# Kernel optimization log

Hardware: AMD Instinct MI355X
Metric: run time of the kernel (lower is better)

## Reference

```python
import jax, jax.numpy as jnp
import numpy as np

B, H, W, D, C, K, ITERS = 16, 64, 64, 64, 16, 5, 4
EPS_LN = 1e-5

def _ln(x, g, b):
    m = x.mean(-1, keepdims=True)
    v = jnp.mean((x - m) ** 2, axis=-1, keepdims=True)
    return (x - m) / jnp.sqrt(v + EPS_LN) * g + b

def _build_grid(h, w):
    # (h, w, 2) with x in [-1,1] over width, y in [-1,1] over height
    y, x = jnp.meshgrid(jnp.linspace(-1.0, 1.0, h), jnp.linspace(-1.0, 1.0, w), indexing='ij')
    return jnp.stack([x, y], axis=-1)

def _forward(feat, feat_color, mask, slot_noise, slots_mu, slots_logsigma,
             w_grid, b_grid, w_k, w_v, ln_kv_g, ln_kv_b, w_mlp, b_mlp,
             ln_q_g, ln_q_b, w_q, w_ih, w_hh, b_ih, b_hh,
             ln_feat_g, ln_feat_b, ln_color_g, ln_color_b,
             ln_res_g, ln_res_b, w_res, b_res):
    b, h, w, d = feat.shape
    n = h * w
    k_slots = mask.shape[0]
    scale = d ** (-0.5)

    grid = _build_grid(h, w)  # (H, W, 2)

    # fg position: weighted mean of grid under mask -> (K, 2), broadcast to (B, K, 2)
    gm = grid.transpose(2, 0, 1)[None] * mask            # (K, 2, H, W)
    fg_pos = gm.sum((2, 3)) / (mask.sum((2, 3)) + 1e-5)  # (K, 2)
    fg_pos = jnp.broadcast_to(fg_pos[None], (b, k_slots, 2))

    feat_n = _ln(feat.reshape(b, n, d), ln_feat_g, ln_feat_b)                    # (B, N, D)
    featc_n = _ln(feat_color.reshape(b, n, feat_color.shape[-1]), ln_color_g, ln_color_b)

    slot = slots_mu + jnp.exp(slots_logsigma) * slot_noise  # (B, K, D)

    # k/v with relative positional grid embedding (fg_pos is constant across iters,
    # so k/v are iteration-invariant and computed once -- same math as the original loop)
    rel = grid[None, None] - fg_pos[:, :, None, None, :]        # (B, K, H, W, 2)
    rel4 = jnp.concatenate([rel, -rel], -1).reshape(b, k_slots, n, 4)
    grid_embed = rel4 @ w_grid.T + b_grid                       # (B, K, N, D)
    k = _ln(feat_n @ w_k.T[None] [0][None][0][None][0] if False else (feat_n @ w_k.T)[:, None] + grid_embed, ln_kv_g, ln_kv_b) @ w_mlp.T + b_mlp
    v = _ln((feat_n @ w_v.T)[:, None] + grid_embed, ln_kv_g, ln_kv_b) @ w_mlp.T + b_mlp

    attn = None
    for it in range(ITERS):
        prev = slot
        q = _ln(slot, ln_q_g, ln_q_b) @ w_q.T                         # (B, K, D)
        logits = jnp.einsum('bkd,bknd->bkn', q, k) * scale
        attn = jax.nn.softmax(logits, axis=-1)                        # (B, K, N)
        upd = jnp.einsum('bkn,bknd->bkd', attn, v)                    # (B, K, D)
        if it != ITERS - 1:
            # torch GRUCell
            x = upd.reshape(-1, d)
            hp = slot.reshape(-1, d)
            gi = x @ w_ih.T + b_ih
            gh = hp @ w_hh.T + b_hh
            i_r, i_z, i_n = jnp.split(gi, 3, axis=-1)
            h_r, h_z, h_n = jnp.split(gh, 3, axis=-1)
            r = jax.nn.sigmoid(i_r + h_r)
            z = jax.nn.sigmoid(i_z + h_z)
            nn_ = jnp.tanh(i_n + r * h_n)
            slot = ((1.0 - z) * nn_ + z * hp).reshape(b, k_slots, d)
            slot = _ln(slot, ln_res_g, ln_res_b) @ w_res.T + b_res + prev
        else:
            slot_color = jnp.einsum('bkn,bnc->bkc', attn, featc_n)
            slot = jnp.concatenate([slot, slot_color], axis=-1)       # (B, K, D+C)

    amin = attn.min(axis=2, keepdims=True)
    amax = attn.max(axis=2, keepdims=True)
    attn = (attn - amin) / (amax - amin + 1e-5)
    return slot, fg_pos, attn

def setup_inputs() -> dict:
    key = jax.random.key(0)
    ks = jax.random.split(key, 16)
    def rn(i, shape, s=0.02):
        return jax.random.normal(ks[i], shape, jnp.float32) * s
    return {
        'feat': jax.random.normal(ks[0], (B, H, W, D), jnp.float32),
        'feat_color': jax.random.normal(ks[1], (B, H, W, C), jnp.float32),
        'mask': jax.random.uniform(ks[2], (K, 1, H, W), jnp.float32),
        'slot_noise': jax.random.normal(ks[3], (B, K, D), jnp.float32),
        'slots_mu': rn(4, (1, 1, D), 1.0),
        'slots_logsigma': rn(5, (1, 1, D), 0.01),
        'w_grid': rn(6, (D, 4)), 'b_grid': jnp.zeros((D,), jnp.float32),
        'w_k': rn(7, (D, D)), 'w_v': rn(8, (D, D)),
        'ln_kv_g': jnp.ones((D,), jnp.float32), 'ln_kv_b': jnp.zeros((D,), jnp.float32),
        'w_mlp': rn(9, (D, D)), 'b_mlp': jnp.zeros((D,), jnp.float32),
        'ln_q_g': jnp.ones((D,), jnp.float32), 'ln_q_b': jnp.zeros((D,), jnp.float32),
        'w_q': rn(10, (D, D)),
        'w_ih': rn(11, (3 * D, D)), 'w_hh': rn(12, (3 * D, D)),
        'b_ih': jnp.zeros((3 * D,), jnp.float32), 'b_hh': jnp.zeros((3 * D,), jnp.float32),
        'ln_feat_g': jnp.ones((D,), jnp.float32), 'ln_feat_b': jnp.zeros((D,), jnp.float32),
        'ln_color_g': jnp.ones((C,), jnp.float32), 'ln_color_b': jnp.zeros((C,), jnp.float32),
        'ln_res_g': jnp.ones((D,), jnp.float32), 'ln_res_b': jnp.zeros((D,), jnp.float32),
        'w_res': rn(13, (D, D)), 'b_res': jnp.zeros((D,), jnp.float32),
    }

def reference(feat, feat_color, mask, slot_noise, slots_mu, slots_logsigma,
              w_grid, b_grid, w_k, w_v, ln_kv_g, ln_kv_b, w_mlp, b_mlp,
              ln_q_g, ln_q_b, w_q, w_ih, w_hh, b_ih, b_hh,
              ln_feat_g, ln_feat_b, ln_color_g, ln_color_b,
              ln_res_g, ln_res_b, w_res, b_res):
    return _forward(feat, feat_color, mask, slot_noise, slots_mu, slots_logsigma,
                    w_grid, b_grid, w_k, w_v, ln_kv_g, ln_kv_b, w_mlp, b_mlp,
                    ln_q_g, ln_q_b, w_q, w_ih, w_hh, b_ih, b_hh,
                    ln_feat_g, ln_feat_b, ln_color_g, ln_color_b,
                    ln_res_g, ln_res_b, w_res, b_res)
```

## Files before the change

kernel.cpp:

```cpp
#include <hip/hip_runtime.h>
#include <stdint.h>

#define B_ 16
#define H_ 64
#define W_ 64
#define D_ 64
#define C_ 16
#define K_ 5
#define N_ 4096
#define NC_ 32
#define CS_ 128
#define EPS 1e-5f

typedef __attribute__((ext_vector_type(8))) short bf16x8;
typedef __attribute__((ext_vector_type(4))) float f32x4;

__device__ __forceinline__ float wsum64(float v){
  #pragma unroll
  for(int o=1;o<64;o<<=1) v += __shfl_xor(v,o,64);
  return v;
}
__device__ __forceinline__ float wmax64(float v){
  #pragma unroll
  for(int o=1;o<64;o<<=1) v = fmaxf(v, __shfl_xor(v,o,64));
  return v;
}
__device__ __forceinline__ float wmin64(float v){
  #pragma unroll
  for(int o=1;o<64;o<<=1) v = fminf(v, __shfl_xor(v,o,64));
  return v;
}
__device__ __forceinline__ uint16_t f2bf(float f){
  uint32_t u = __float_as_uint(f);
  u += 0x7fffu + ((u>>16)&1u);
  return (uint16_t)(u>>16);
}

__global__ __launch_bounds__(256) void k_pre(
    const float* __restrict__ mask, const float* __restrict__ noise,
    const float* __restrict__ mu, const float* __restrict__ lsg,
    const float* __restrict__ wm, const float* __restrict__ bm, const float* __restrict__ lnkb,
    const float* __restrict__ wk, const float* __restrict__ wv, const float* __restrict__ lnfb,
    const float* __restrict__ wq, const float* __restrict__ lnqg, const float* __restrict__ lnqb,
    const float* __restrict__ wres, const float* __restrict__ bres,
    const float* __restrict__ lnrg, const float* __restrict__ lnrb,
    const float* __restrict__ wih, const float* __restrict__ whh,
    const float* __restrict__ wg, const float* __restrict__ bg,
    const float* __restrict__ lnfg, const float* __restrict__ lnkg,
    float* __restrict__ ws_fg, float* __restrict__ out_fg,
    float* __restrict__ bm2, float* __restrict__ fkb, float* __restrict__ fvb,
    float* __restrict__ qb, float* __restrict__ br2,
    float* __restrict__ wgx, float* __restrict__ wgy, float* __restrict__ gscal,
    float* __restrict__ wqpT, float* __restrict__ wrpT,
    float* __restrict__ wvT, float* __restrict__ wmT,
    float* __restrict__ gw, float* __restrict__ slot, float* __restrict__ out_slot,
    float* __restrict__ WQp, float* __restrict__ WCp, float* __restrict__ bq2p,
    float* __restrict__ uvp, float* __restrict__ vqp, float* __restrict__ cscp){
  __shared__ float M0[64][65];
  __shared__ float M1[64][65];
  __shared__ float M2[64][65];
  __shared__ float vtmp[4][64];
  int bid=blockIdx.x, tid=threadIdx.x;
  if(bid<5){
    int k=bid;
    float sm=0.f, sx=0.f, sy=0.f;
    for(int p=tid; p<H_*W_; p+=256){
      int i=p>>6, j=p&63;
      float m = mask[k*H_*W_ + p];
      float x = -1.f + (2.f/63.f)*j;
      float y = -1.f + (2.f/63.f)*i;
      sm+=m; sx+=m*x; sy+=m*y;
    }
    __shared__ float r0[4], r1[4], r2[4];
    int wid=tid>>6, lane=tid&63;
    sm=wsum64(sm); sx=wsum64(sx); sy=wsum64(sy);
    if(lane==0){ r0[wid]=sm; r1[wid]=sx; r2[wid]=sy; }
    __syncthreads();
    if(tid==0){
      float tm=r0[0]+r0[1]+r0[2]+r0[3];
      float tx=r1[0]+r1[1]+r1[2]+r1[3];
      float ty=r2[0]+r2[1]+r2[2]+r2[3];
      float px = tx/(tm+1e-5f), py = ty/(tm+1e-5f);
      ws_fg[k*2+0]=px; ws_fg[k*2+1]=py;
      for(int b=0;b<B_;b++){ out_fg[(b*K_+k)*2+0]=px; out_fg[(b*K_+k)*2+1]=py; }
    }
  } else if(bid==5){
    int sel=tid>>6, o=tid&63; float s=0.f;
    if(sel==0){ s=bm[o]; for(int d=0;d<64;d++) s+=lnkb[d]*wm[o*64+d]; bm2[o]=s; }
    else if(sel==1){ for(int d=0;d<64;d++) s+=lnqb[d]*wq[o*64+d]; qb[o]=0.125f*s; }
    else if(sel==2){ for(int d=0;d<64;d++) s+=lnrb[d]*wres[o*64+d]; br2[o]=s+bres[o]; }
    else { for(int d=0;d<64;d++) s+=lnfb[d]*wk[o*64+d]; fkb[o]=s; }
  } else if(bid==6){
    int wv4=tid>>6, l=tid&63;
    if(wv4==0){ float s=0.f; for(int d=0;d<64;d++) s+=lnfb[d]*wv[l*64+d]; fvb[l]=s; }
    else if(wv4==1){
      float4 w4 = *(const float4*)(wg + l*4);
      wgx[l]=w4.x-w4.z; wgy[l]=w4.y-w4.w;
    } else if(wv4==2){
      float4 w4 = *(const float4*)(wg + l*4);
      float wx=w4.x-w4.z, wy=w4.y-w4.w, bl=bg[l];
      float t;
      t=wsum64(wx);    if(l==0) gscal[0]=t*(1.f/64.f);
      t=wsum64(wy);    if(l==0) gscal[1]=t*(1.f/64.f);
      t=wsum64(bl);    if(l==0) gscal[2]=t*(1.f/64.f);
      t=wsum64(wx*wx); if(l==0) gscal[3]=t*(1.f/64.f);
      t=wsum64(wy*wy); if(l==0) gscal[4]=t*(1.f/64.f);
      t=wsum64(wx*wy); if(l==0) gscal[5]=t*(2.f/64.f);
      t=wsum64(wx*bl); if(l==0) gscal[6]=t*(2.f/64.f);
      t=wsum64(wy*bl); if(l==0) gscal[7]=t*(2.f/64.f);
      t=wsum64(bl*bl); if(l==0) gscal[8]=t*(1.f/64.f);
    } else {
      for(int j=l;j<B_*K_*16;j+=64){ int bk2=j>>4, cc2=j&15; out_slot[bk2*80+64+cc2]=0.f; }
    }
  } else if(bid<71){
    int i=(bid-7)*256+tid;
    int a=i>>12, r=i&4095, d=r>>6, o=r&63;
    if(a==0)      wqpT[r]=0.125f*lnqg[d]*wq[o*64+d];
    else if(a==1) wrpT[r]=lnrg[d]*wres[o*64+d];
    else if(a==2) wvT[r]=wv[o*64+d];
    else          wmT[r]=wm[o*64+d];
  } else if(bid<167){
    int i=(bid-71)*256+tid;
    int g6=i>>12, r=i&4095, d=r>>6, o=r&63;
    float v = (g6<3)? wih[(g6*64+o)*64+d] : whh[((g6-3)*64+o)*64+d];
    gw[g6*4096 + d*64 + o] = v;
  } else if(bid<187){
    int i=(bid-167)*256+tid;
    if(i<B_*K_*D_){ int d=i&63; slot[i]=mu[d]+expf(lsg[d])*noise[i]; }
  } else if(bid==187){
    for(int i=tid;i<4096;i+=256){ int r=i>>6,c2=i&63; M0[r][c2]=wq[i]; M1[r][c2]=wm[i]; }
    __syncthreads();
    if(tid<64){ float s=0.f; for(int d=0;d<64;d++) s+=lnqb[d]*M0[tid][d]; vtmp[0][tid]=0.125f*s; }
    else if(tid<128){ int c2=tid-64; float s=bm[c2]; for(int d=0;d<64;d++) s+=lnkb[d]*M1[c2][d]; vtmp[1][c2]=s; }
    else if(tid<192){ int o=tid-128; float s=0.f; for(int d=0;d<64;d++) s+=lnfb[d]*wk[o*64+d]; vtmp[2][o]=s; }
    __syncthreads();
    for(int i=tid;i<4096;i+=256){ int d=i>>6,e=i&63; float s=0.f;
      for(int c2=0;c2<64;c2++) s=fmaf(M0[c2][d], M1[c2][e], s);
      M2[d][e]=0.125f*lnqg[d]*s; }
    __syncthreads();
    if(tid<64){
      int e=tid; float s=0.f; for(int c2=0;c2<64;c2++) s=fmaf(vtmp[0][c2], M1[c2][e], s); vtmp[3][e]=s;
    } else if(tid<128){
      int d=tid-64; float s=0.f; for(int c2=0;c2<64;c2++) s=fmaf(M0[c2][d], vtmp[1][c2], s);
      vqp[4*64+d]=0.125f*lnqg[d]*s;
    }
    __syncthreads();
    for(int i=tid;i<4096;i+=256){ int e=i>>6,o=i&63; M0[e][o]=lnkg[e]*wk[i]; }
    __syncthreads();
    for(int i=tid;i<4096;i+=256){ int d=i>>6,o=i&63; float s=0.f;
      for(int e=0;e<64;e++) s=fmaf(M2[d][e], M0[e][o], s);
      WQp[i]=lnfg[o]*s; }
    if(tid<64){ int o=tid; float s=0.f;
      for(int e=0;e<64;e++) s=fmaf(vtmp[3][e], M0[e][o], s);
      bq2p[o]=lnfg[o]*s; }
    else if(tid<128){ int d=tid-64; float s1=0.f,sx=0.f,sy=0.f,s3=0.f;
      for(int e=0;e<64;e++){ float pe=M2[d][e]*lnkg[e];
        float gx_=wg[e*4]-wg[e*4+2], gy_=wg[e*4+1]-wg[e*4+3];
        s1+=pe; sx+=pe*gx_; sy+=pe*gy_; s3+=pe*(bg[e]+vtmp[2][e]); }
      vqp[0*64+d]=s1; vqp[1*64+d]=sx; vqp[2*64+d]=sy; vqp[3*64+d]=s3; }
    else if(tid==128){ float c0=0.f,c1=0.f,c2=0.f,c3=0.f,c4=0.f;
      for(int e=0;e<64;e++){ float qe=vtmp[3][e]*lnkg[e];
        float gx_=wg[e*4]-wg[e*4+2], gy_=wg[e*4+1]-wg[e*4+3];
        c0+=qe; c1+=qe*gx_; c2+=qe*gy_; c3+=qe*(bg[e]+vtmp[2][e]);
        c4+=vtmp[0][e]*vtmp[1][e]; }
      cscp[0]=c0; cscp[1]=c1; cscp[2]=c2; cscp[3]=c3; cscp[4]=c4; }
  } else {
    for(int i=tid;i<4096;i+=256){ int r=i>>6,c2=i&63; M0[r][c2]=wv[i]*lnkg[r]; M1[r][c2]=wm[i]; }
    __syncthreads();
    if(tid<64){ float s=0.f; const float* wr=wv+tid*64;
      for(int d=0;d<64;d++) s+=lnfb[d]*wr[d]; vtmp[0][tid]=s; }
    __syncthreads();
    for(int i=tid;i<4096;i+=256){ int d=i>>6,o=i&63; float s=0.f;
      for(int e=0;e<64;e++) s=fmaf(M0[e][d], M1[o][e], s);
      WCp[i]=lnfg[d]*s; }
    if(tid<64){ int o=tid; float s1=0.f,s2=0.f,s3=0.f,s4=0.f;
      for(int e=0;e<64;e++){ float we=lnkg[e]*M1[o][e];
        float gx_=wg[e*4]-wg[e*4+2], gy_=wg[e*4+1]-wg[e*4+3];
        s1+=we*(vtmp[0][e]+bg[e]); s2+=we*gx_; s3+=we*gy_; s4+=we; }
      uvp[0*64+o]=s1; uvp[1*64+o]=s2; uvp[2*64+o]=s3; uvp[3*64+o]=s4; }
  }
}

__global__ __launch_bounds__(256) void k_featln(const float* __restrict__ feat,
    const float* __restrict__ wk, const float* __restrict__ wv, const float* __restrict__ gf,
    const float* __restrict__ fkb, const float* __restrict__ fvb,
    const float* __restrict__ wgx, const float* __restrict__ wgy, const float* __restrict__ bg,
    const float* __restrict__ fc, const float* __restrict__ gc, const float* __restrict__ bc,
    uint16_t* __restrict__ Aout, float4* __restrict__ kstat, float4* __restrict__ vstat,
    float* __restrict__ fcn){
  int tid=threadIdx.x, wid=tid>>6, lane=tid&63;
  int q=lane>>4, c=lane&15;
  size_t row = (size_t)blockIdx.x*64 + wid*16 + c;
  const float* xp = feat + row*64;
  float x[16];
  *(float4*)&x[0]  = *(const float4*)(xp + q*8);
  *(float4*)&x[4]  = *(const float4*)(xp + q*8 + 4);
  *(float4*)&x[8]  = *(const float4*)(xp + 32 + q*8);
  *(float4*)&x[12] = *(const float4*)(xp + 36 + q*8);
  float s=0.f;
  #pragma unroll
  for(int i=0;i<16;i++) s+=x[i];
  s += __shfl_xor(s,16,64); s += __shfl_xor(s,32,64);
  float mean = s*(1.f/64.f);
  float v=0.f;
  #pragma unroll
  for(int i=0;i<16;i++){ float d=x[i]-mean; v+=d*d; }
  v += __shfl_xor(v,16,64); v += __shfl_xor(v,32,64);
  float rs = rsqrtf(v*(1.f/64.f)+EPS);
  float gl[16];
  *(float4*)&gl[0]  = *(const float4*)(gf + q*8);
  *(float4*)&gl[4]  = *(const float4*)(gf + q*8 + 4);
  *(float4*)&gl[8]  = *(const float4*)(gf + 32 + q*8);
  *(float4*)&gl[12] = *(const float4*)(gf + 36 + q*8);
  bf16x8 A0, A1;
  #pragma unroll
  for(int j=0;j<8;j++){
    A0[j] = (short)f2bf((x[j]  -mean)*rs);
    A1[j] = (short)f2bf((x[8+j]-mean)*rs);
  }
  *(bf16x8*)(Aout + row*64 + q*8) = A0;
  *(bf16x8*)(Aout + row*64 + 32 + q*8) = A1;
  float wgxl[4][4], wgyl[4][4], bgl[4][4];
  #pragma unroll
  for(int ot=0;ot<4;ot++){
    *(float4*)&wgxl[ot][0] = *(const float4*)(wgx + ot*16 + q*4);
    *(float4*)&wgyl[ot][0] = *(const float4*)(wgy + ot*16 + q*4);
    *(float4*)&bgl[ot][0]  = *(const float4*)(bg + ot*16 + q*4);
  }
  #pragma unroll
  for(int mat=0;mat<2;mat++){
    const float* w = mat? wv : wk;
    const float* fb = mat? fvb : fkb;
    float ss=0.f, s2=0.f, dx=0.f, dy=0.f, db=0.f;
    #pragma unroll
    for(int ot=0; ot<4; ot++){
      const float* wp = w + (size_t)(ot*16+c)*64 + q*8;
      bf16x8 W0, W1;
      #pragma unroll
      for(int j=0;j<8;j++){ W0[j]=(short)f2bf(wp[j]*gl[j]); W1[j]=(short)f2bf(wp[32+j]*gl[8+j]); }
      float4 bq = *(const float4*)(fb + ot*16 + q*4);
      f32x4 acc = {bq.x,bq.y,bq.z,bq.w};
      acc = __builtin_amdgcn_mfma_f32_16x16x32_bf16(W0, A0, acc, 0,0,0);
      acc = __builtin_amdgcn_mfma_f32_16x16x32_bf16(W1, A1, acc, 0,0,0);
      #pragma unroll
      for(int r=0;r<4;r++){
        float a=acc[r];
        ss+=a; s2+=a*a;
        dx = fmaf(a, wgxl[ot][r], dx);
        dy = fmaf(a, wgyl[ot][r], dy);
        db = fmaf(a, bgl[ot][r], db);
      }
    }
    ss += __shfl_xor(ss,16,64); ss += __shfl_xor(ss,32,64);
    s2 += __shfl_xor(s2,16,64); s2 += __shfl_xor(s2,32,64);
    dx += __shfl_xor(dx,16,64); dx += __shfl_xor(dx,32,64);
    dy += __shfl_xor(dy,16,64); dy += __shfl_xor(dy,32,64);
    db += __shfl_xor(db,16,64); db += __shfl_xor(db,32,64);
    if(lane<16){
      size_t row2 = (size_t)blockIdx.x*64 + wid*16 + lane;
      float4 st = { ss*(1.f/64.f), s2*(1.f/64.f)+db*(1.f/32.f), dx*(1.f/32.f), dy*(1.f/32.f) };
      (mat? vstat : kstat)[row2] = st;
    }
  }
  int r16=tid>>4, cc=tid&15;
  #pragma unroll
  for(int i=0;i<4;i++){
    size_t row2 = (size_t)blockIdx.x*64 + i*16 + r16;
    float xv = fc[row2*16+cc];
    float sc=xv;
    #pragma unroll
    for(int o=1;o<16;o<<=1) sc += __shfl_xor(sc,o,16);
    float m2 = sc*(1.f/16.f);
    float df = xv-m2;
    float v2 = df*df;
    #pragma unroll
    for(int o=1;o<16;o<<=1) v2 += __shfl_xor(v2,o,16);
    fcn[row2*16+cc] = df*rsqrtf(v2*(1.f/16.f)+EPS)*gc[cc] + bc[cc];
  }
}

#define MV5(W) { \
  float p0=0.f,p1=0.f,p2=0.f,p3=0.f,p4=0.f; \
  _Pragma("unroll") \
  for(int d4=0;d4<4;d4++){ \
    int d0_=wid*16+d4*4; \
    float4 q0_=*(const float4*)&sq[0][d0_]; \
    float4 q1_=*(const float4*)&sq[1][d0_]; \
    float4 q2_=*(const float4*)&sq[2][d0_]; \
    float4 q3_=*(const float4*)&sq[3][d0_]; \
    float4 q4_=*(const float4*)&sq[4][d0_]; \
    float w0_=(W)[(d0_+0)*64+lane]; \
    float w1_=(W)[(d0_+1)*64+lane]; \
    float w2_=(W)[(d0_+2)*64+lane]; \
    float w3_=(W)[(d0_+3)*64+lane]; \
    p0=fmaf(q0_.x,w0_,p0); p0=fmaf(q0_.y,w1_,p0); p0=fmaf(q0_.z,w2_,p0); p0=fmaf(q0_.w,w3_,p0); \
    p1=fmaf(q1_.x,w0_,p1); p1=fmaf(q1_.y,w1_,p1); p1=fmaf(q1_.z,w2_,p1); p1=fmaf(q1_.w,w3_,p1); \
    p2=fmaf(q2_.x,w0_,p2); p2=fmaf(q2_.y,w1_,p2); p2=fmaf(q2_.z,w2_,p2); p2=fmaf(q2_.w,w3_,p2); \
    p3=fmaf(q3_.x,w0_,p3); p3=fmaf(q3_.y,w1_,p3); p3=fmaf(q3_.z,w2_,p3); p3=fmaf(q3_.w,w3_,p3); \
    p4=fmaf(q4_.x,w0_,p4); p4=fmaf(q4_.y,w1_,p4); p4=fmaf(q4_.z,w2_,p4); p4=fmaf(q4_.w,w3_,p4); \
  } \
  redp[wid][lane][0]=p0; redp[wid][lane][1]=p1; redp[wid][lane][2]=p2; \
  redp[wid][lane][3]=p3; redp[wid][lane][4]=p4; \
  __syncthreads(); }

template<bool GRU, bool FINAL>
__global__ __launch_bounds__(256,2) void k_attn(const uint16_t* __restrict__ Aw,
    const float4* __restrict__ kstat, const float4* __restrict__ vstat,
    const float* __restrict__ gscal, const float* __restrict__ ws_fg,
    const float* __restrict__ slot_prev, float* __restrict__ slot_cur,
    const float* __restrict__ part_in, const float* __restrict__ pscal_in,
    const float* __restrict__ red_in,
    const float* __restrict__ gw, const float* __restrict__ bih, const float* __restrict__ bhh,
    const float* __restrict__ wrpT, const float* __restrict__ br2, const float* __restrict__ bm2,
    const float* __restrict__ WQ, const float* __restrict__ bq2,
    const float* __restrict__ WC, const float* __restrict__ uvec,
    const float* __restrict__ vq, const float* __restrict__ csc,
    float* __restrict__ lgt, float* __restrict__ red_out,
    float* __restrict__ part_o, float* __restrict__ pscal_o){
  __shared__ uint32_t As_[CS_*32];
  __shared__ __align__(16) float dps[5][CS_+4];
  __shared__ float pw[4][5][64];
  __shared__ float rm[2][5], rn[2][5];
  __shared__ float rsc[2][5][5];
  __shared__ float cstl[5][5];
  __shared__ float fgl[5][2];
  __shared__ __align__(16) float sq[5][64];
  __shared__ float xg[5][64];
  __shared__ float hg[5][64];
  __shared__ float redp[4][64][5];
  __shared__ float lamS[5][NC_];
  __shared__ float scal4[5][4];
  int chunk=blockIdx.x, b=blockIdx.y;
  int tid=threadIdx.x, wid=tid>>6, lane=tid&63;
  int c=lane&15, q=lane>>4;
  int bk0=b*K_;
  float mwgx=gscal[0], mwgy=gscal[1], mbg=gscal[2];
  float g1=gscal[3], g2=gscal[4], g3=gscal[5], g4=gscal[6], g5=gscal[7], g6=gscal[8];
  if(tid<10) fgl[tid>>1][tid&1]=ws_fg[tid];
  bool act = tid < CS_;
  int nrow = chunk*CS_ + (tid & (CS_-1));
  float4 st, sv;
  float gx=0.f, gy=0.f;
  if(act){
    st = kstat[(size_t)b*N_ + nrow];
    if(!FINAL) sv = vstat[(size_t)b*N_ + nrow];
    gx = -1.f + (2.f/63.f)*(nrow&63);
    gy = -1.f + (2.f/63.f)*(nrow>>6);
  }

  if(GRU){
    for(int s=wid; s<5; s+=4){
      size_t base=(size_t)(bk0+s)*NC_;
      float m_l=(lane<NC_)? red_in[(base+lane)*4]   : -1e30f;
      float s_l=(lane<NC_)? red_in[(base+lane)*4+1] : 0.f;
      float M=wmax64(m_l);
      float eu=(lane<NC_)? __expf(m_l-M) : 0.f;
      float S=wsum64(s_l*eu);
      float lam=eu/S;
      if(lane<NC_) lamS[s][lane]=lam;
      float p0=(lane<NC_)? pscal_in[(base+lane)*4+0]:0.f;
      float p1=(lane<NC_)? pscal_in[(base+lane)*4+1]:0.f;
      float p2=(lane<NC_)? pscal_in[(base+lane)*4+2]:0.f;
      float p3=(lane<NC_)? pscal_in[(base+lane)*4+3]:0.f;
      float As=wsum64(lam*p0), Ax=wsum64(lam*p1), Ay=wsum64(lam*p2), Am=wsum64(lam*p3);
      if(lane==0){ scal4[s][0]=As; scal4[s][1]=Ax; scal4[s][2]=Ay; scal4[s][3]=Am; }
    }
    __syncthreads();
    #pragma unroll
    for(int s=0;s<5;s++){
      float p_=0.f;
      #pragma unroll
      for(int j=0;j<8;j++){
        int cc=wid*8+j;
        p_=fmaf(lamS[s][cc], part_in[((size_t)(bk0+s)*NC_+cc)*64+lane], p_);
      }
      redp[wid][lane][s]=p_;
    }
    __syncthreads();
    for(int s=wid; s<5; s+=4)
      sq[s][lane]=redp[0][lane][s]+redp[1][lane][s]+redp[2][lane][s]+redp[3][lane][s];
    __syncthreads();
    MV5(WC);
    for(int s=wid; s<5; s+=4){
      float As=scal4[s][0],Ax=scal4[s][1],Ay=scal4[s][2],Am=scal4[s][3];
      float x_=redp[0][lane][s]+redp[1][lane][s]+redp[2][lane][s]+redp[3][lane][s]
              + As*uvec[lane] + Ax*uvec[64+lane] + Ay*uvec[128+lane] - Am*uvec[192+lane]
              + bm2[lane];
      xg[s][lane]=x_;
      hg[s][lane]=slot_prev[(bk0+s)*64+lane];
    }
    __syncthreads();
    {
      float pr[5]={0,0,0,0,0}, pz[5]={0,0,0,0,0}, pi[5]={0,0,0,0,0}, ph[5]={0,0,0,0,0};
      #pragma unroll
      for(int dd=0;dd<16;dd++){
        int d=wid*16+dd;
        float g0_=gw[d*64+lane],       g1_=gw[4096+d*64+lane],  g2_=gw[8192+d*64+lane];
        float g3_=gw[12288+d*64+lane], g4_=gw[16384+d*64+lane], g5_=gw[20480+d*64+lane];
        #pragma unroll
        for(int s=0;s<5;s++){
          float xd=xg[s][d], hd=hg[s][d];
          pr[s]=fmaf(xd,g0_,pr[s]); pr[s]=fmaf(hd,g3_,pr[s]);
          pz[s]=fmaf(xd,g1_,pz[s]); pz[s]=fmaf(hd,g4_,pz[s]);
          pi[s]=fmaf(xd,g2_,pi[s]);
          ph[s]=fmaf(hd,g5_,ph[s]);
        }
      }
      float* redG=(float*)As_;
      #pragma unroll
      for(int s=0;s<4;s++){
        redG[(s*4+0)*256+tid]=pr[s];
        redG[(s*4+1)*256+tid]=pz[s];
        redG[(s*4+2)*256+tid]=pi[s];
        redG[(s*4+3)*256+tid]=ph[s];
      }
      redp[wid][lane][0]=pr[4]; redp[wid][lane][1]=pz[4];
      redp[wid][lane][2]=pi[4]; redp[wid][lane][3]=ph[4];
    }
    __syncthreads();
    for(int s=wid; s<5; s+=4){
      const float* redG=(const float*)As_;
      float pr_,pz_,pi_,ph_;
      if(s<4){
        int b0=(s*4+0)*256, b1=(s*4+1)*256, b2=(s*4+2)*256, b3=(s*4+3)*256;
        pr_=redG[b0+lane]+redG[b0+64+lane]+redG[b0+128+lane]+redG[b0+192+lane];
        pz_=redG[b1+lane]+redG[b1+64+lane]+redG[b1+128+lane]+redG[b1+192+lane];
        pi_=redG[b2+lane]+redG[b2+64+lane]+redG[b2+128+lane]+redG[b2+192+lane];
        ph_=redG[b3+lane]+redG[b3+64+lane]+redG[b3+128+lane]+redG[b3+192+lane];
      } else {
        pr_=redp[0][lane][0]+redp[1][lane][0]+redp[2][lane][0]+redp[3][lane][0];
        pz_=redp[0][lane][1]+redp[1][lane][1]+redp[2][lane][1]+redp[3][lane][1];
        pi_=redp[0][lane][2]+redp[1][lane][2]+redp[2][lane][2]+redp[3][lane][2];
        ph_=redp[0][lane][3]+redp[1][lane][3]+redp[2][lane][3]+redp[3][lane][3];
      }
      float r=1.f/(1.f+__expf(-(pr_+bih[lane]+bhh[lane])));
      float z=1.f/(1.f+__expf(-(pz_+bih[64+lane]+bhh[64+lane])));
      float nn=tanhf(pi_+bih[128+lane] + r*(ph_+bhh[128+lane]));
      float hp=hg[s][lane];
      float sp=(1.f-z)*nn+z*hp;
      float m=wsum64(sp)*(1.f/64.f);
      float df=sp-m;
      float var=wsum64(df*df)*(1.f/64.f);
      sq[s][lane]=df*rsqrtf(var+EPS);
    }
    __syncthreads();
    MV5(wrpT);
    for(int s=wid; s<5; s+=4){
      float cur=redp[0][lane][s]+redp[1][lane][s]+redp[2][lane][s]+redp[3][lane][s]
               + br2[lane] + hg[s][lane];
      if(chunk==0) slot_cur[(bk0+s)*64+lane]=cur;
      float m=wsum64(cur)*(1.f/64.f);
      float df=cur-m;
      float var=wsum64(df*df)*(1.f/64.f);
      float LNc=df*rsqrtf(var+EPS);
      sq[s][lane]=LNc;
      float s1=wsum64(LNc*vq[lane])     + csc[0];
      float c1=wsum64(LNc*vq[64+lane])  + csc[1];
      float c2=wsum64(LNc*vq[128+lane]) + csc[2];
      float c3=wsum64(LNc*vq[192+lane]) + csc[3];
      float c4=wsum64(LNc*vq[256+lane]) + csc[4];
      if(lane==0){
        cstl[s][0]=c1-s1*mwgx; cstl[s][1]=c2-s1*mwgy; cstl[s][2]=c3-s1*mbg;
        cstl[s][3]=s1; cstl[s][4]=c4;
      }
    }
    __syncthreads();
  } else {
    for(int s=wid; s<5; s+=4){
      float cur=slot_prev[(bk0+s)*64+lane];
      float m=wsum64(cur)*(1.f/64.f);
      float df=cur-m;
      float var=wsum64(df*df)*(1.f/64.f);
      float LNc=df*rsqrtf(var+EPS);
      sq[s][lane]=LNc;
      float s1=wsum64(LNc*vq[lane])     + csc[0];
      float c1=wsum64(LNc*vq[64+lane])  + csc[1];
      float c2=wsum64(LNc*vq[128+lane]) + csc[2];
      float c3=wsum64(LNc*vq[192+lane]) + csc[3];
      float c4=wsum64(LNc*vq[256+lane]) + csc[4];
      if(lane==0){
        cstl[s][0]=c1-s1*mwgx; cstl[s][1]=c2-s1*mwgy; cstl[s][2]=c3-s1*mbg;
        cstl[s][3]=s1; cstl[s][4]=c4;
      }
    }
    __syncthreads();
  }
  MV5(WQ);
  for(int s=wid; s<5; s+=4)
    xg[s][lane]=redp[0][lane][s]+redp[1][lane][s]+redp[2][lane][s]+redp[3][lane][s] + bq2[lane];
  __syncthreads();

  if(!FINAL){
    const uint4* Ag = (const uint4*)(Aw + ((size_t)b*N_ + chunk*CS_)*64);
    #pragma unroll
    for(int jj=0;jj<4;jj++){
      int f = jj*256 + tid;
      *(uint4*)(As_ + f*4) = Ag[f];
    }
  }

  {
    bf16x8 QF0={0,0,0,0,0,0,0,0}, QF1={0,0,0,0,0,0,0,0};
    if(c<5){
      const float* qpp = &xg[c][0];
      #pragma unroll
      for(int j=0;j<8;j++){
        QF0[j] = (short)f2bf(qpp[q*8+j]);
        QF1[j] = (short)f2bf(qpp[32+q*8+j]);
      }
    }
    const uint16_t* Abase = Aw + ((size_t)b*N_ + chunk*CS_)*64;
    #pragma unroll
    for(int it=0;it<2;it++){
      int tile = wid*32 + it*16;
      const uint16_t* rp = Abase + (size_t)(tile+c)*64;
      bf16x8 BF0 = *(const bf16x8*)(rp + q*8);
      bf16x8 BF1 = *(const bf16x8*)(rp + 32 + q*8);
      f32x4 acc = {0.f,0.f,0.f,0.f};
      acc = __builtin_amdgcn_mfma_f32_16x16x32_bf16(QF0, BF0, acc, 0,0,0);
      acc = __builtin_amdgcn_mfma_f32_16x16x32_bf16(QF1, BF1, acc, 0,0,0);
      #pragma unroll
      for(int r=0;r<4;r++){
        int s = q*4+r;
        if(s<5) dps[s][tile+c]=acc[r];
      }
    }
  }
  __syncthreads();

  float l5[5], w5[5];
  if(act){
    #pragma unroll
    for(int k=0;k<5;k++){
      float rx = gx - fgl[k][0], ry = gy - fgl[k][1];
      float CX=cstl[k][0], CY=cstl[k][1], C0=cstl[k][2], S1=cstl[k][3], C4=cstl[k][4];
      float quad = g1*rx*rx + g2*ry*ry + g3*rx*ry + g4*rx + g5*ry + g6;
      float mu = st.x + rx*mwgx + ry*mwgy + mbg;
      float var = st.y + rx*st.z + ry*st.w + quad - mu*mu;
      float rsn = rsqrtf(var+EPS);
      float l = rsn*(dps[k][tid] + rx*CX + ry*CY + C0 - S1*st.x) + C4;
      l5[k]=l;
      float wmx = wmax64(l);
      if(lane==0) rm[wid][k]=wmx;
      if(FINAL){ float mn=wmin64(l); if(lane==0) rn[wid][k]=mn; }
    }
  }
  __syncthreads();
  if(act){
    #pragma unroll
    for(int k=0;k<5;k++){
      float m_c = fmaxf(rm[0][k], rm[1][k]);
      float e = __expf(l5[k]-m_c);
      float scq = wsum64(e);
      if(!FINAL){
        float rx = gx - fgl[k][0], ry = gy - fgl[k][1];
        float quad = g1*rx*rx + g2*ry*ry + g3*rx*ry + g4*rx + g5*ry + g6;
        float muV = sv.x + rx*mwgx + ry*mwgy + mbg;
        float varV = sv.y + rx*sv.z + ry*sv.w + quad - muV*muV;
        float rsv_ = rsqrtf(varV+EPS);
        float w_ = e*rsv_;
        w5[k]=w_;
        float As2=wsum64(w_), Ax2=wsum64(w_*rx), Ay2=wsum64(w_*ry), Am2=wsum64(w_*muV);
        if(lane==0){ rsc[wid][k][0]=scq; rsc[wid][k][1]=As2; rsc[wid][k][2]=Ax2;
                     rsc[wid][k][3]=Ay2; rsc[wid][k][4]=Am2; }
      } else {
        lgt[(size_t)(bk0+k)*N_ + nrow] = l5[k];
        if(lane==0) rsc[wid][k][0]=scq;
      }
    }
  }
  __syncthreads();
  if(tid<5){
    int k=tid;
    size_t idx = ((size_t)(bk0+k)*NC_+chunk)*4;
    red_out[idx+0]=fmaxf(rm[0][k],rm[1][k]);
    red_out[idx+1]=rsc[0][k][0]+rsc[1][k][0];
    if(FINAL) red_out[idx+2]=fminf(rn[0][k],rn[1][k]);
    if(!FINAL){
      pscal_o[idx+0]=rsc[0][k][1]+rsc[1][k][1];
      pscal_o[idx+1]=rsc[0][k][2]+rsc[1][k][2];
      pscal_o[idx+2]=rsc[0][k][3]+rsc[1][k][3];
      pscal_o[idx+3]=rsc[0][k][4]+rsc[1][k][4];
    }
  }
  if(act && !FINAL){
    #pragma unroll
    for(int k=0;k<5;k++) dps[k][tid]=w5[k];
  }

  if(!FINAL){
    __syncthreads();
    const uint16_t* Au = (const uint16_t*)As_;
    float a0=0.f,a1=0.f,a2=0.f,a3=0.f,a4=0.f;
    #pragma unroll
    for(int rb=0;rb<8;rb++){
      int row0 = wid*32 + rb*4;
      float4 d0 = *(const float4*)&dps[0][row0];
      float4 d1 = *(const float4*)&dps[1][row0];
      float4 d2 = *(const float4*)&dps[2][row0];
      float4 d3 = *(const float4*)&dps[3][row0];
      float4 d4 = *(const float4*)&dps[4][row0];
      float av0 = __uint_as_float(((uint32_t)Au[(row0+0)*64+lane])<<16);
      float av1 = __uint_as_float(((uint32_t)Au[(row0+1)*64+lane])<<16);
      float av2 = __uint_as_float(((uint32_t)Au[(row0+2)*64+lane])<<16);
      float av3 = __uint_as_float(((uint32_t)Au[(row0+3)*64+lane])<<16);
      a0=fmaf(d0.x,av0,a0); a0=fmaf(d0.y,av1,a0); a0=fmaf(d0.z,av2,a0); a0=fmaf(d0.w,av3,a0);
      a1=fmaf(d1.x,av0,a1); a1=fmaf(d1.y,av1,a1); a1=fmaf(d1.z,av2,a1); a1=fmaf(d1.w,av3,a1);
      a2=fmaf(d2.x,av0,a2); a2=fmaf(d2.y,av1,a2); a2=fmaf(d2.z,av2,a2); a2=fmaf(d2.w,av3,a2);
      a3=fmaf(d3.x,av0,a3); a3=fmaf(d3.y,av1,a3); a3=fmaf(d3.z,av2,a3); a3=fmaf(d3.w,av3,a3);
      a4=fmaf(d4.x,av0,a4); a4=fmaf(d4.y,av1,a4); a4=fmaf(d4.z,av2,a4); a4=fmaf(d4.w,av3,a4);
    }
    pw[wid][0][lane]=a0; pw[wid][1][lane]=a1; pw[wid][2][lane]=a2;
    pw[wid][3][lane]=a3; pw[wid][4][lane]=a4;
    __syncthreads();
    if(tid<64){
      #pragma unroll
      for(int k=0;k<5;k++){
        float s2 = pw[0][k][tid]+pw[1][k][tid]+pw[2][k][tid]+pw[3][k][tid];
        part_o[((size_t)(bk0+k)*NC_+chunk)*64 + tid] = s2;
      }
    }
  }
}

__global__ __launch_bounds__(256) void k_fin(const float* __restrict__ lgt,
    const float* __restrict__ red, const float* __restrict__ featc,
    const float* __restrict__ sl1, float* __restrict__ out_slot,
    float* __restrict__ out_attn){
  __shared__ float psp[CS_];
  __shared__ float pcz[4][16];
  int chunk=blockIdx.x, bk=blockIdx.y, b=bk/K_;
  int tid=threadIdx.x, wid=tid>>6, lane=tid&63, sub=lane>>4, c4=lane&15;
  const float* rp = red + (size_t)bk*NC_*4;
  float M=-1e30f;
  #pragma unroll
  for(int i=0;i<NC_;i++) M = fmaxf(M, rp[i*4]);
  float S=0.f;
  #pragma unroll
  for(int i=0;i<NC_;i++) S += rp[i*4+1]*__expf(rp[i*4]-M);
  float invS = 1.f/S;
  float LMIN=1e30f;
  #pragma unroll
  for(int i=0;i<NC_;i++) LMIN=fminf(LMIN, rp[i*4+2]);
  float amin = __expf(LMIN-M)*invS;
  float dinv = 1.f/(invS - amin + 1e-5f);
  const float* lp = lgt + (size_t)bk*N_ + chunk*CS_;
  if(tid<CS_){
    float p = __expf(lp[tid]-M)*invS;
    psp[tid]=p;
    out_attn[(size_t)bk*N_ + chunk*CS_ + tid] = (p - amin)*dinv;
  }
  __syncthreads();
  const float* Fb = featc + ((size_t)b*N_ + chunk*CS_)*16;
  float ac=0.f;
  for(int t=0;t<8;t++){
    int n = wid*32 + t*4 + sub;
    ac += psp[n]*Fb[(size_t)n*16 + c4];
  }
  ac+=__shfl_xor(ac,16,64); ac+=__shfl_xor(ac,32,64);
  if(lane<16) pcz[wid][lane]=ac;
  __syncthreads();
  if(tid<16){
    float s2 = pcz[0][tid]+pcz[1][tid]+pcz[2][tid]+pcz[3][tid];
    atomicAdd(&out_slot[bk*80+64+tid], s2);
  }
  if(chunk==0 && tid<64) out_slot[bk*80+tid]=sl1[bk*64+tid];
}

extern "C" void kernel_launch(void* const* d_in, const int* in_sizes, int n_in,
                              void* d_out, int out_size, void* d_ws, size_t ws_size,
                              hipStream_t stream){
  (void)in_sizes; (void)n_in; (void)out_size; (void)ws_size;
  const float* feat = (const float*)d_in[0];
  const float* featc= (const float*)d_in[1];
  const float* mask = (const float*)d_in[2];
  const float* noise= (const float*)d_in[3];
  const float* mu   = (const float*)d_in[4];
  const float* lsg  = (const float*)d_in[5];
  const float* wg   = (const float*)d_in[6];
  const float* bg   = (const float*)d_in[7];
  const float* wk   = (const float*)d_in[8];
  const float* wv   = (const float*)d_in[9];
  const float* lnkg = (const float*)d_in[10];
  const float* lnkb = (const float*)d_in[11];
  const float* wm   = (const float*)d_in[12];
  const float* bm   = (const float*)d_in[13];
  const float* lnqg = (const float*)d_in[14];
  const float* lnqb = (const float*)d_in[15];
  const float* wq   = (const float*)d_in[16];
  const float* wih  = (const float*)d_in[17];
  const float* whh  = (const float*)d_in[18];
  const float* bih  = (const float*)d_in[19];
  const float* bhh  = (const float*)d_in[20];
  const float* lnfg = (const float*)d_in[21];
  const float* lnfb = (const float*)d_in[22];
  const float* lncg = (const float*)d_in[23];
  const float* lncb = (const float*)d_in[24];
  const float* lnrg = (const float*)d_in[25];
  const float* lnrb = (const float*)d_in[26];
  const float* wres = (const float*)d_in[27];
  const float* bres = (const float*)d_in[28];

  float* out = (float*)d_out;
  float* out_slot = out;
  float* out_fg   = out + 6400;
  float* out_attn = out + 6560;

  float* wsf     = (float*)d_ws;
  float* ws_fg   = wsf;
  float* ws_bm2  = wsf + 16;
  float* ws_fkb  = ws_bm2 + 64;
  float* ws_fvb  = ws_fkb + 64;
  float* ws_qb   = ws_fvb + 64;
  float* ws_br2  = ws_qb + 64;
  float* ws_wgx  = ws_br2 + 64;
  float* ws_wgy  = ws_wgx + 64;
  float* ws_gs   = ws_wgy + 64;
  float* ws_wqpT = ws_gs + 16;
  float* ws_wrpT = ws_wqpT + 4096;
  float* ws_wvT  = ws_wrpT + 4096;
  float* ws_wmT  = ws_wvT + 4096;
  float* ws_gw   = ws_wmT + 4096;
  float* ws_WQ   = ws_gw + 24576;
  float* ws_WC   = ws_WQ + 4096;
  float* ws_bq2  = ws_WC + 4096;
  float* ws_u    = ws_bq2 + 64;
  float* ws_vq   = ws_u + 256;
  float* ws_csc  = ws_vq + 320;
  float* ws_fc   = ws_csc + 16;
  float* ws_sl0  = ws_fc + (size_t)B_*N_*C_;
  float* ws_sl1  = ws_sl0 + B_*K_*D_;
  float* ws_lgt  = ws_sl1 + B_*K_*D_;
  float* ws_red0 = ws_lgt + (size_t)B_*K_*N_;
  float* ws_red1 = ws_red0 + B_*K_*NC_*4;
  float* ws_prt0 = ws_red1 + B_*K_*NC_*4;
  float* ws_prt1 = ws_prt0 + (size_t)B_*K_*NC_*64;
  float* ws_psc0 = ws_prt1 + (size_t)B_*K_*NC_*64;
  float* ws_psc1 = ws_psc0 + B_*K_*NC_*4;
  float4* ws_kst = (float4*)(ws_psc1 + B_*K_*NC_*4);
  float4* ws_vst = ws_kst + (size_t)B_*N_;
  uint16_t* ws_A = (uint16_t*)(ws_vst + (size_t)B_*N_);

  k_pre<<<189,256,0,stream>>>(mask,noise,mu,lsg, wm,bm,lnkb, wk,wv,lnfb,
                              wq,lnqg,lnqb, wres,bres,lnrg,lnrb, wih,whh, wg,bg,
                              lnfg,lnkg,
                              ws_fg,out_fg, ws_bm2,ws_fkb,ws_fvb,ws_qb,ws_br2,
                              ws_wgx,ws_wgy,ws_gs,
                              ws_wqpT,ws_wrpT,ws_wvT,ws_wmT, ws_gw, ws_sl0, out_slot,
                              ws_WQ, ws_WC, ws_bq2, ws_u, ws_vq, ws_csc);
  k_featln<<<(B_*N_)/64,256,0,stream>>>(feat,wk,wv,lnfg,ws_fkb,ws_fvb,
                                        ws_wgx,ws_wgy,bg,
                                        featc,lncg,lncb,
                                        ws_A,ws_kst,ws_vst,ws_fc);

  dim3 agrid(NC_,B_);
  #define ATT_COMMON ws_A,ws_kst,ws_vst,ws_gs,ws_fg
  #define ATT_W ws_gw,bih,bhh,ws_wrpT,ws_br2,ws_bm2,ws_WQ,ws_bq2,ws_WC,ws_u,ws_vq,ws_csc

  k_attn<false,false><<<agrid,256,0,stream>>>(ATT_COMMON, ws_sl0, ws_sl1,
      ws_prt1, ws_psc1, ws_red1, ATT_W, ws_lgt, ws_red0, ws_prt0, ws_psc0);
  k_attn<true,false><<<agrid,256,0,stream>>>(ATT_COMMON, ws_sl0, ws_sl1,
      ws_prt0, ws_psc0, ws_red0, ATT_W, ws_lgt, ws_red1, ws_prt1, ws_psc1);
  k_attn<true,false><<<agrid,256,0,stream>>>(ATT_COMMON, ws_sl1, ws_sl0,
      ws_prt1, ws_psc1, ws_red1, ATT_W, ws_lgt, ws_red0, ws_prt0, ws_psc0);
  k_attn<true,true><<<agrid,256,0,stream>>>(ATT_COMMON, ws_sl0, ws_sl1,
      ws_prt0, ws_psc0, ws_red0, ATT_W, ws_lgt, ws_red1, ws_prt1, ws_psc1);
  k_fin<<<dim3(NC_,B_*K_),256,0,stream>>>(ws_lgt,ws_red1,ws_fc,ws_sl1,out_slot,out_attn);
}
```

Baseline: 258.5 us.

## Move GRU slot update into last-block tail of attention kernel via atomic counter

Restructures the iteration schedule. Each attention kernel previously began with a redundant per-block GRU/slot update and query projection. Now a per-batch atomic counter elects the last-finishing block to do the GRU, residual MLP and next-iteration query projection once, writing q and scalar constants to workspace. A small new kernel computes the first-iteration query, and k_pre's weight products are rewritten as 4x4 register-tiled matmuls with some dead transposes dropped. This removes the duplicated prologue work across all blocks, but adds a serialized tail in one block per batch and depends on counter and memory-ordering correctness.

```diff
diff --git a/kernel.cpp b/kernel.cpp
--- a/kernel.cpp
+++ b/kernel.cpp
@@ -35,6 +35,30 @@
   u += 0x7fffu + ((u>>16)&1u);
   return (uint16_t)(u>>16);
 }
+
+#define MV5(W) { \
+  float p0=0.f,p1=0.f,p2=0.f,p3=0.f,p4=0.f; \
+  _Pragma("unroll") \
+  for(int d4=0;d4<4;d4++){ \
+    int d0_=wid*16+d4*4; \
+    float4 q0_=*(const float4*)&sq[0][d0_]; \
+    float4 q1_=*(const float4*)&sq[1][d0_]; \
+    float4 q2_=*(const float4*)&sq[2][d0_]; \
+    float4 q3_=*(const float4*)&sq[3][d0_]; \
+    float4 q4_=*(const float4*)&sq[4][d0_]; \
+    float w0_=(W)[(d0_+0)*64+lane]; \
+    float w1_=(W)[(d0_+1)*64+lane]; \
+    float w2_=(W)[(d0_+2)*64+lane]; \
+    float w3_=(W)[(d0_+3)*64+lane]; \
+    p0=fmaf(q0_.x,w0_,p0); p0=fmaf(q0_.y,w1_,p0); p0=fmaf(q0_.z,w2_,p0); p0=fmaf(q0_.w,w3_,p0); \
+    p1=fmaf(q1_.x,w0_,p1); p1=fmaf(q1_.y,w1_,p1); p1=fmaf(q1_.z,w2_,p1); p1=fmaf(q1_.w,w3_,p1); \
+    p2=fmaf(q2_.x,w0_,p2); p2=fmaf(q2_.y,w1_,p2); p2=fmaf(q2_.z,w2_,p2); p2=fmaf(q2_.w,w3_,p2); \
+    p3=fmaf(q3_.x,w0_,p3); p3=fmaf(q3_.y,w1_,p3); p3=fmaf(q3_.z,w2_,p3); p3=fmaf(q3_.w,w3_,p3); \
+    p4=fmaf(q4_.x,w0_,p4); p4=fmaf(q4_.y,w1_,p4); p4=fmaf(q4_.z,w2_,p4); p4=fmaf(q4_.w,w3_,p4); \
+  } \
+  redp[wid][lane][0]=p0; redp[wid][lane][1]=p1; redp[wid][lane][2]=p2; \
+  redp[wid][lane][3]=p3; redp[wid][lane][4]=p4; \
+  __syncthreads(); }
 
 __global__ __launch_bounds__(256) void k_pre(
     const float* __restrict__ mask, const float* __restrict__ noise,
@@ -51,16 +75,28 @@
     float* __restrict__ bm2, float* __restrict__ fkb, float* __restrict__ fvb,
     float* __restrict__ qb, float* __restrict__ br2,
     float* __restrict__ wgx, float* __restrict__ wgy, float* __restrict__ gscal,
-    float* __restrict__ wqpT, float* __restrict__ wrpT,
-    float* __restrict__ wvT, float* __restrict__ wmT,
+    float* __restrict__ wrpT,
     float* __restrict__ gw, float* __restrict__ slot, float* __restrict__ out_slot,
     float* __restrict__ WQp, float* __restrict__ WCp, float* __restrict__ bq2p,
-    float* __restrict__ uvp, float* __restrict__ vqp, float* __restrict__ cscp){
-  __shared__ float M0[64][65];
-  __shared__ float M1[64][65];
-  __shared__ float M2[64][65];
+    float* __restrict__ uvp, float* __restrict__ vqp, float* __restrict__ cscp,
+    int* __restrict__ cntp){
+  __shared__ __align__(16) float M0[64][68];
+  __shared__ __align__(16) float M1[64][68];
+  __shared__ __align__(16) float M2T[64][68];
   __shared__ float vtmp[4][64];
+  __shared__ float aux[4][64];
   int bid=blockIdx.x, tid=threadIdx.x;
+
+  #define MM44(SRCA, SRCB) { \
+    float a4[4], b4[4]; \
+    *(float4*)a4 = *(const float4*)(SRCA); \
+    *(float4*)b4 = *(const float4*)(SRCB); \
+    _Pragma("unroll") \
+    for(int ii=0;ii<4;ii++){ \
+      _Pragma("unroll") \
+      for(int jj=0;jj<4;jj++) acc[ii][jj]=fmaf(a4[ii],b4[jj],acc[ii][jj]); \
+    } }
+
   if(bid<5){
     int k=bid;
     float sm=0.f, sx=0.f, sy=0.f;
@@ -111,32 +147,44 @@
       t=wsum64(bl*bl); if(l==0) gscal[8]=t*(1.f/64.f);
     } else {
       for(int j=l;j<B_*K_*16;j+=64){ int bk2=j>>4, cc2=j&15; out_slot[bk2*80+64+cc2]=0.f; }
-    }
-  } else if(bid<71){
+      if(l<48) cntp[l]=0;
+    }
+  } else if(bid<23){
     int i=(bid-7)*256+tid;
-    int a=i>>12, r=i&4095, d=r>>6, o=r&63;
-    if(a==0)      wqpT[r]=0.125f*lnqg[d]*wq[o*64+d];
-    else if(a==1) wrpT[r]=lnrg[d]*wres[o*64+d];
-    else if(a==2) wvT[r]=wv[o*64+d];
-    else          wmT[r]=wm[o*64+d];
-  } else if(bid<167){
-    int i=(bid-71)*256+tid;
+    int d=i>>6, o=i&63;
+    wrpT[i]=lnrg[d]*wres[o*64+d];
+  } else if(bid<119){
+    int i=(bid-23)*256+tid;
     int g6=i>>12, r=i&4095, d=r>>6, o=r&63;
     float v = (g6<3)? wih[(g6*64+o)*64+d] : whh[((g6-3)*64+o)*64+d];
     gw[g6*4096 + d*64 + o] = v;
-  } else if(bid<187){
-    int i=(bid-167)*256+tid;
+  } else if(bid<139){
+    int i=(bid-119)*256+tid;
     if(i<B_*K_*D_){ int d=i&63; slot[i]=mu[d]+expf(lsg[d])*noise[i]; }
-  } else if(bid==187){
+  } else if(bid==139){
     for(int i=tid;i<4096;i+=256){ int r=i>>6,c2=i&63; M0[r][c2]=wq[i]; M1[r][c2]=wm[i]; }
+    if(tid>=192){ int l=tid-192;
+      float4 w4 = *(const float4*)(wg + l*4);
+      aux[0][l]=w4.x-w4.z; aux[1][l]=w4.y-w4.w; aux[2][l]=bg[l]; aux[3][l]=lnkg[l];
+    }
     __syncthreads();
     if(tid<64){ float s=0.f; for(int d=0;d<64;d++) s+=lnqb[d]*M0[tid][d]; vtmp[0][tid]=0.125f*s; }
     else if(tid<128){ int c2=tid-64; float s=bm[c2]; for(int d=0;d<64;d++) s+=lnkb[d]*M1[c2][d]; vtmp[1][c2]=s; }
     else if(tid<192){ int o=tid-128; float s=0.f; for(int d=0;d<64;d++) s+=lnfb[d]*wk[o*64+d]; vtmp[2][o]=s; }
     __syncthreads();
-    for(int i=tid;i<4096;i+=256){ int d=i>>6,e=i&63; float s=0.f;
-      for(int c2=0;c2<64;c2++) s=fmaf(M0[c2][d], M1[c2][e], s);
-      M2[d][e]=0.125f*lnqg[d]*s; }
+    {
+      int d0=(tid>>4)*4, e0=(tid&15)*4;
+      float acc[4][4]={};
+      for(int c2=0;c2<64;c2++) MM44(&M0[c2][d0], &M1[c2][e0]);
+      float lq4[4]; *(float4*)lq4 = *(const float4*)(lnqg+d0);
+      #pragma unroll
+      for(int jj=0;jj<4;jj++){
+        float w4[4];
+        #pragma unroll
+        for(int ii=0;ii<4;ii++) w4[ii]=0.125f*lq4[ii]*acc[ii][jj];
+        *(float4*)&M2T[e0+jj][d0] = *(float4*)w4;
+      }
+    }
     __syncthreads();
     if(tid<64){
       int e=tid; float s=0.f; for(int c2=0;c2<64;c2++) s=fmaf(vtmp[0][c2], M1[c2][e], s); vtmp[3][e]=s;
@@ -145,40 +193,67 @@
       vqp[4*64+d]=0.125f*lnqg[d]*s;
     }
     __syncthreads();
-    for(int i=tid;i<4096;i+=256){ int e=i>>6,o=i&63; M0[e][o]=lnkg[e]*wk[i]; }
-    __syncthreads();
-    for(int i=tid;i<4096;i+=256){ int d=i>>6,o=i&63; float s=0.f;
-      for(int e=0;e<64;e++) s=fmaf(M2[d][e], M0[e][o], s);
-      WQp[i]=lnfg[o]*s; }
+    for(int i=tid;i<4096;i+=256){ int e=i>>6,o=i&63; M0[e][o]=aux[3][e]*wk[i]; }
+    __syncthreads();
+    {
+      int d0=(tid>>4)*4, o0=(tid&15)*4;
+      float acc[4][4]={};
+      for(int e=0;e<64;e++) MM44(&M2T[e][d0], &M0[e][o0]);
+      float lf4[4]; *(float4*)lf4 = *(const float4*)(lnfg+o0);
+      #pragma unroll
+      for(int ii=0;ii<4;ii++){
+        float w4[4];
+        #pragma unroll
+        for(int jj=0;jj<4;jj++) w4[jj]=lf4[jj]*acc[ii][jj];
+        *(float4*)(WQp + (d0+ii)*64 + o0) = *(float4*)w4;
+      }
+    }
     if(tid<64){ int o=tid; float s=0.f;
       for(int e=0;e<64;e++) s=fmaf(vtmp[3][e], M0[e][o], s);
       bq2p[o]=lnfg[o]*s; }
     else if(tid<128){ int d=tid-64; float s1=0.f,sx=0.f,sy=0.f,s3=0.f;
-      for(int e=0;e<64;e++){ float pe=M2[d][e]*lnkg[e];
-        float gx_=wg[e*4]-wg[e*4+2], gy_=wg[e*4+1]-wg[e*4+3];
-        s1+=pe; sx+=pe*gx_; sy+=pe*gy_; s3+=pe*(bg[e]+vtmp[2][e]); }
+      for(int e=0;e<64;e++){ float pe=M2T[e][d]*aux[3][e];
+        s1+=pe; sx+=pe*aux[0][e]; sy+=pe*aux[1][e]; s3+=pe*(aux[2][e]+vtmp[2][e]); }
       vqp[0*64+d]=s1; vqp[1*64+d]=sx; vqp[2*64+d]=sy; vqp[3*64+d]=s3; }
-    else if(tid==128){ float c0=0.f,c1=0.f,c2=0.f,c3=0.f,c4=0.f;
-      for(int e=0;e<64;e++){ float qe=vtmp[3][e]*lnkg[e];
-        float gx_=wg[e*4]-wg[e*4+2], gy_=wg[e*4+1]-wg[e*4+3];
-        c0+=qe; c1+=qe*gx_; c2+=qe*gy_; c3+=qe*(bg[e]+vtmp[2][e]);
-        c4+=vtmp[0][e]*vtmp[1][e]; }
-      cscp[0]=c0; cscp[1]=c1; cscp[2]=c2; cscp[3]=c3; cscp[4]=c4; }
+    else if(tid<192){
+      int e=tid-128;
+      float qe=vtmp[3][e]*aux[3][e];
+      float c0=wsum64(qe);
+      float c1=wsum64(qe*aux[0][e]);
+      float c2=wsum64(qe*aux[1][e]);
+      float c3=wsum64(qe*(aux[2][e]+vtmp[2][e]));
+      float c4=wsum64(vtmp[0][e]*vtmp[1][e]);
+      if(e==0){ cscp[0]=c0; cscp[1]=c1; cscp[2]=c2; cscp[3]=c3; cscp[4]=c4; }
+    }
   } else {
-    for(int i=tid;i<4096;i+=256){ int r=i>>6,c2=i&63; M0[r][c2]=wv[i]*lnkg[r]; M1[r][c2]=wm[i]; }
+    for(int i=tid;i<4096;i+=256){ int r=i>>6,c2=i&63; M0[r][c2]=wv[i]*lnkg[r]; M1[c2][r]=wm[i]; }
+    if(tid>=192){ int l=tid-192;
+      float4 w4 = *(const float4*)(wg + l*4);
+      aux[0][l]=w4.x-w4.z; aux[1][l]=w4.y-w4.w; aux[2][l]=bg[l]; aux[3][l]=lnkg[l];
+    }
     __syncthreads();
     if(tid<64){ float s=0.f; const float* wr=wv+tid*64;
       for(int d=0;d<64;d++) s+=lnfb[d]*wr[d]; vtmp[0][tid]=s; }
     __syncthreads();
-    for(int i=tid;i<4096;i+=256){ int d=i>>6,o=i&63; float s=0.f;
-      for(int e=0;e<64;e++) s=fmaf(M0[e][d], M1[o][e], s);
-      WCp[i]=lnfg[d]*s; }
+    {
+      int d0=(tid>>4)*4, o0=(tid&15)*4;
+      float acc[4][4]={};
+      for(int e=0;e<64;e++) MM44(&M0[e][d0], &M1[e][o0]);
+      float lf4[4]; *(float4*)lf4 = *(const float4*)(lnfg+d0);
+      #pragma unroll
+      for(int ii=0;ii<4;ii++){
+        float w4[4];
+        #pragma unroll
+        for(int jj=0;jj<4;jj++) w4[jj]=lf4[ii]*acc[ii][jj];
+        *(float4*)(WCp + (d0+ii)*64 + o0) = *(float4*)w4;
+      }
+    }
     if(tid<64){ int o=tid; float s1=0.f,s2=0.f,s3=0.f,s4=0.f;
-      for(int e=0;e<64;e++){ float we=lnkg[e]*M1[o][e];
-        float gx_=wg[e*4]-wg[e*4+2], gy_=wg[e*4+1]-wg[e*4+3];
-        s1+=we*(vtmp[0][e]+bg[e]); s2+=we*gx_; s3+=we*gy_; s4+=we; }
+      for(int e=0;e<64;e++){ float we=aux[3][e]*M1[e][o];
+        s1+=we*(vtmp[0][e]+aux[2][e]); s2+=we*aux[0][e]; s3+=we*aux[1][e]; s4+=we; }
       uvp[0*64+o]=s1; uvp[1*64+o]=s2; uvp[2*64+o]=s3; uvp[3*64+o]=s4; }
   }
+  #undef MM44
 }
 
 __global__ __launch_bounds__(256) void k_featln(const float* __restrict__ feat,
@@ -279,44 +354,58 @@
   }
 }
 
-#define MV5(W) { \
-  float p0=0.f,p1=0.f,p2=0.f,p3=0.f,p4=0.f; \
-  _Pragma("unroll") \
-  for(int d4=0;d4<4;d4++){ \
-    int d0_=wid*16+d4*4; \
-    float4 q0_=*(const float4*)&sq[0][d0_]; \
-    float4 q1_=*(const float4*)&sq[1][d0_]; \
-    float4 q2_=*(const float4*)&sq[2][d0_]; \
-    float4 q3_=*(const float4*)&sq[3][d0_]; \
-    float4 q4_=*(const float4*)&sq[4][d0_]; \
-    float w0_=(W)[(d0_+0)*64+lane]; \
-    float w1_=(W)[(d0_+1)*64+lane]; \
-    float w2_=(W)[(d0_+2)*64+lane]; \
-    float w3_=(W)[(d0_+3)*64+lane]; \
-    p0=fmaf(q0_.x,w0_,p0); p0=fmaf(q0_.y,w1_,p0); p0=fmaf(q0_.z,w2_,p0); p0=fmaf(q0_.w,w3_,p0); \
-    p1=fmaf(q1_.x,w0_,p1); p1=fmaf(q1_.y,w1_,p1); p1=fmaf(q1_.z,w2_,p1); p1=fmaf(q1_.w,w3_,p1); \
-    p2=fmaf(q2_.x,w0_,p2); p2=fmaf(q2_.y,w1_,p2); p2=fmaf(q2_.z,w2_,p2); p2=fmaf(q2_.w,w3_,p2); \
-    p3=fmaf(q3_.x,w0_,p3); p3=fmaf(q3_.y,w1_,p3); p3=fmaf(q3_.z,w2_,p3); p3=fmaf(q3_.w,w3_,p3); \
-    p4=fmaf(q4_.x,w0_,p4); p4=fmaf(q4_.y,w1_,p4); p4=fmaf(q4_.z,w2_,p4); p4=fmaf(q4_.w,w3_,p4); \
-  } \
-  redp[wid][lane][0]=p0; redp[wid][lane][1]=p1; redp[wid][lane][2]=p2; \
-  redp[wid][lane][3]=p3; redp[wid][lane][4]=p4; \
-  __syncthreads(); }
-
-template<bool GRU, bool FINAL>
-__global__ __launch_bounds__(256,2) void k_attn(const uint16_t* __restrict__ Aw,
+__global__ __launch_bounds__(256) void k_slotq0(
+    const float* __restrict__ slot_prev,
+    const float* __restrict__ WQ, const float* __restrict__ bq2,
+    const float* __restrict__ vq, const float* __restrict__ csc,
+    const float* __restrict__ gscal,
+    float* __restrict__ qs_out, float* __restrict__ cst_out){
+  __shared__ float vv[64];
+  __shared__ float red4[4][64];
+  int bk=blockIdx.x;
+  int tid=threadIdx.x, wid=tid>>6, lane=tid&63;
+  int o=lane, qq=wid;
+  float mwgx=gscal[0], mwgy=gscal[1], mbg=gscal[2];
+  float cur=0.f;
+  if(wid==0) cur = slot_prev[bk*64+lane];
+  if(wid==0){
+    float m=wsum64(cur)*(1.f/64.f); float df=cur-m;
+    float var=wsum64(df*df)*(1.f/64.f);
+    float LNc=df*rsqrtf(var+EPS);
+    vv[lane]=LNc;
+    float s1=wsum64(LNc*vq[lane])     + csc[0];
+    float c1=wsum64(LNc*vq[64+lane])  + csc[1];
+    float c2=wsum64(LNc*vq[128+lane]) + csc[2];
+    float c3=wsum64(LNc*vq[192+lane]) + csc[3];
+    float c4=wsum64(LNc*vq[256+lane]) + csc[4];
+    if(lane==0){
+      float* cp = cst_out + bk*8;
+      cp[0]=c1-s1*mwgx; cp[1]=c2-s1*mwgy; cp[2]=c3-s1*mbg; cp[3]=s1; cp[4]=c4;
+    }
+  }
+  __syncthreads();
+  { float p_=0.f;
+    #pragma unroll
+    for(int dd=0;dd<16;dd++) p_ = fmaf(vv[qq*16+dd], WQ[(qq*16+dd)*64+o], p_);
+    red4[qq][o]=p_; }
+  __syncthreads();
+  if(wid==0) qs_out[bk*64+lane] = red4[0][lane]+red4[1][lane]+red4[2][lane]+red4[3][lane] + bq2[lane];
+}
+
+template<bool FINAL, bool GRUTAIL>
+__global__ __launch_bounds__(256) void k_attn(const uint16_t* __restrict__ Aw,
     const float4* __restrict__ kstat, const float4* __restrict__ vstat,
+    float* qs, float* cst,
     const float* __restrict__ gscal, const float* __restrict__ ws_fg,
+    float* __restrict__ lgt, float* __restrict__ red_out,
+    float* __restrict__ part_o, float* __restrict__ pscal_o,
     const float* __restrict__ slot_prev, float* __restrict__ slot_cur,
-    const float* __restrict__ part_in, const float* __restrict__ pscal_in,
-    const float* __restrict__ red_in,
     const float* __restrict__ gw, const float* __restrict__ bih, const float* __restrict__ bhh,
     const float* __restrict__ wrpT, const float* __restrict__ br2, const float* __restrict__ bm2,
     const float* __restrict__ WQ, const float* __restrict__ bq2,
     const float* __restrict__ WC, const float* __restrict__ uvec,
     const float* __restrict__ vq, const float* __restrict__ csc,
-    float* __restrict__ lgt, float* __restrict__ red_out,
-    float* __restrict__ part_o, float* __restrict__ pscal_o){
+    int* cnt){
   __shared__ uint32_t As_[CS_*32];
   __shared__ __align__(16) float dps[5][CS_+4];
   __shared__ float pw[4][5][64];
@@ -324,19 +413,22 @@
   __shared__ float rsc[2][5][5];
   __shared__ float cstl[5][5];
   __shared__ float fgl[5][2];
-  __shared__ __align__(16) float sq[5][64];
-  __shared__ float xg[5][64];
-  __shared__ float hg[5][64];
-  __shared__ float redp[4][64][5];
-  __shared__ float lamS[5][NC_];
-  __shared__ float scal4[5][4];
   int chunk=blockIdx.x, b=blockIdx.y;
   int tid=threadIdx.x, wid=tid>>6, lane=tid&63;
   int c=lane&15, q=lane>>4;
-  int bk0=b*K_;
   float mwgx=gscal[0], mwgy=gscal[1], mbg=gscal[2];
   float g1=gscal[3], g2=gscal[4], g3=gscal[5], g4=gscal[6], g5=gscal[7], g6=gscal[8];
-  if(tid<10) fgl[tid>>1][tid&1]=ws_fg[tid];
+
+  if(!FINAL){
+    const uint4* Ag = (const uint4*)(Aw + ((size_t)b*N_ + chunk*CS_)*64);
+    #pragma unroll
+    for(int jj=0;jj<4;jj++){
+      int f = jj*256 + tid;
+      *(uint4*)(As_ + f*4) = Ag[f];
+    }
+  }
+  if(tid<25) cstl[tid/5][tid%5] = cst[(b*K_ + tid/5)*8 + (tid%5)];
+  if(tid>=32 && tid<42){ int i2=tid-32; fgl[i2>>1][i2&1] = ws_fg[i2]; }
   bool act = tid < CS_;
   int nrow = chunk*CS_ + (tid & (CS_-1));
   float4 st, sv;
@@ -347,162 +439,12 @@
     gx = -1.f + (2.f/63.f)*(nrow&63);
     gy = -1.f + (2.f/63.f)*(nrow>>6);
   }
-
-  if(GRU){
-    for(int s=wid; s<5; s+=4){
-      size_t base=(size_t)(bk0+s)*NC_;
-      float m_l=(lane<NC_)? red_in[(base+lane)*4]   : -1e30f;
-      float s_l=(lane<NC_)? red_in[(base+lane)*4+1] : 0.f;
-      float M=wmax64(m_l);
-      float eu=(lane<NC_)? __expf(m_l-M) : 0.f;
-      float S=wsum64(s_l*eu);
-      float lam=eu/S;
-      if(lane<NC_) lamS[s][lane]=lam;
-      float p0=(lane<NC_)? pscal_in[(base+lane)*4+0]:0.f;
-      float p1=(lane<NC_)? pscal_in[(base+lane)*4+1]:0.f;
-      float p2=(lane<NC_)? pscal_in[(base+lane)*4+2]:0.f;
-      float p3=(lane<NC_)? pscal_in[(base+lane)*4+3]:0.f;
-      float As=wsum64(lam*p0), Ax=wsum64(lam*p1), Ay=wsum64(lam*p2), Am=wsum64(lam*p3);
-      if(lane==0){ scal4[s][0]=As; scal4[s][1]=Ax; scal4[s][2]=Ay; scal4[s][3]=Am; }
-    }
-    __syncthreads();
-    #pragma unroll
-    for(int s=0;s<5;s++){
-      float p_=0.f;
-      #pragma unroll
-      for(int j=0;j<8;j++){
-        int cc=wid*8+j;
-        p_=fmaf(lamS[s][cc], part_in[((size_t)(bk0+s)*NC_+cc)*64+lane], p_);
-      }
-      redp[wid][lane][s]=p_;
-    }
-    __syncthreads();
-    for(int s=wid; s<5; s+=4)
-      sq[s][lane]=redp[0][lane][s]+redp[1][lane][s]+redp[2][lane][s]+redp[3][lane][s];
-    __syncthreads();
-    MV5(WC);
-    for(int s=wid; s<5; s+=4){
-      float As=scal4[s][0],Ax=scal4[s][1],Ay=scal4[s][2],Am=scal4[s][3];
-      float x_=redp[0][lane][s]+redp[1][lane][s]+redp[2][lane][s]+redp[3][lane][s]
-              + As*uvec[lane] + Ax*uvec[64+lane] + Ay*uvec[128+lane] - Am*uvec[192+lane]
-              + bm2[lane];
-      xg[s][lane]=x_;
-      hg[s][lane]=slot_prev[(bk0+s)*64+lane];
-    }
-    __syncthreads();
-    {
-      float pr[5]={0,0,0,0,0}, pz[5]={0,0,0,0,0}, pi[5]={0,0,0,0,0}, ph[5]={0,0,0,0,0};
-      #pragma unroll
-      for(int dd=0;dd<16;dd++){
-        int d=wid*16+dd;
-        float g0_=gw[d*64+lane],       g1_=gw[4096+d*64+lane],  g2_=gw[8192+d*64+lane];
-        float g3_=gw[12288+d*64+lane], g4_=gw[16384+d*64+lane], g5_=gw[20480+d*64+lane];
-        #pragma unroll
-        for(int s=0;s<5;s++){
-          float xd=xg[s][d], hd=hg[s][d];
-          pr[s]=fmaf(xd,g0_,pr[s]); pr[s]=fmaf(hd,g3_,pr[s]);
-          pz[s]=fmaf(xd,g1_,pz[s]); pz[s]=fmaf(hd,g4_,pz[s]);
-          pi[s]=fmaf(xd,g2_,pi[s]);
-          ph[s]=fmaf(hd,g5_,ph[s]);
-        }
-      }
-      float* redG=(float*)As_;
-      #pragma unroll
-      for(int s=0;s<4;s++){
-        redG[(s*4+0)*256+tid]=pr[s];
-        redG[(s*4+1)*256+tid]=pz[s];
-        redG[(s*4+2)*256+tid]=pi[s];
-        redG[(s*4+3)*256+tid]=ph[s];
-      }
-      redp[wid][lane][0]=pr[4]; redp[wid][lane][1]=pz[4];
-      redp[wid][lane][2]=pi[4]; redp[wid][lane][3]=ph[4];
-    }
-    __syncthreads();
-    for(int s=wid; s<5; s+=4){
-      const float* redG=(const float*)As_;
-      float pr_,pz_,pi_,ph_;
-      if(s<4){
-        int b0=(s*4+0)*256, b1=(s*4+1)*256, b2=(s*4+2)*256, b3=(s*4+3)*256;
-        pr_=redG[b0+lane]+redG[b0+64+lane]+redG[b0+128+lane]+redG[b0+192+lane];
-        pz_=redG[b1+lane]+redG[b1+64+lane]+redG[b1+128+lane]+redG[b1+192+lane];
-        pi_=redG[b2+lane]+redG[b2+64+lane]+redG[b2+128+lane]+redG[b2+192+lane];
-        ph_=redG[b3+lane]+redG[b3+64+lane]+redG[b3+128+lane]+redG[b3+192+lane];
-      } else {
-        pr_=redp[0][lane][0]+redp[1][lane][0]+redp[2][lane][0]+redp[3][lane][0];
-        pz_=redp[0][lane][1]+redp[1][lane][1]+redp[2][lane][1]+redp[3][lane][1];
-        pi_=redp[0][lane][2]+redp[1][lane][2]+redp[2][lane][2]+redp[3][lane][2];
-        ph_=redp[0][lane][3]+redp[1][lane][3]+redp[2][lane][3]+redp[3][lane][3];
-      }
-      float r=1.f/(1.f+__expf(-(pr_+bih[lane]+bhh[lane])));
-      float z=1.f/(1.f+__expf(-(pz_+bih[64+lane]+bhh[64+lane])));
-      float nn=tanhf(pi_+bih[128+lane] + r*(ph_+bhh[128+lane]));
-      float hp=hg[s][lane];
-      float sp=(1.f-z)*nn+z*hp;
-      float m=wsum64(sp)*(1.f/64.f);
-      float df=sp-m;
-      float var=wsum64(df*df)*(1.f/64.f);
-      sq[s][lane]=df*rsqrtf(var+EPS);
-    }
-    __syncthreads();
-    MV5(wrpT);
-    for(int s=wid; s<5; s+=4){
-      float cur=redp[0][lane][s]+redp[1][lane][s]+redp[2][lane][s]+redp[3][lane][s]
-               + br2[lane] + hg[s][lane];
-      if(chunk==0) slot_cur[(bk0+s)*64+lane]=cur;
-      float m=wsum64(cur)*(1.f/64.f);
-      float df=cur-m;
-      float var=wsum64(df*df)*(1.f/64.f);
-      float LNc=df*rsqrtf(var+EPS);
-      sq[s][lane]=LNc;
-      float s1=wsum64(LNc*vq[lane])     + csc[0];
-      float c1=wsum64(LNc*vq[64+lane])  + csc[1];
-      float c2=wsum64(LNc*vq[128+lane]) + csc[2];
-      float c3=wsum64(LNc*vq[192+lane]) + csc[3];
-      float c4=wsum64(LNc*vq[256+lane]) + csc[4];
-      if(lane==0){
-        cstl[s][0]=c1-s1*mwgx; cstl[s][1]=c2-s1*mwgy; cstl[s][2]=c3-s1*mbg;
-        cstl[s][3]=s1; cstl[s][4]=c4;
-      }
-    }
-    __syncthreads();
-  } else {
-    for(int s=wid; s<5; s+=4){
-      float cur=slot_prev[(bk0+s)*64+lane];
-      float m=wsum64(cur)*(1.f/64.f);
-      float df=cur-m;
-      float var=wsum64(df*df)*(1.f/64.f);
-      float LNc=df*rsqrtf(var+EPS);
-      sq[s][lane]=LNc;
-      float s1=wsum64(LNc*vq[lane])     + csc[0];
-      float c1=wsum64(LNc*vq[64+lane])  + csc[1];
-      float c2=wsum64(LNc*vq[128+lane]) + csc[2];
-      float c3=wsum64(LNc*vq[192+lane]) + csc[3];
-      float c4=wsum64(LNc*vq[256+lane]) + csc[4];
-      if(lane==0){
-        cstl[s][0]=c1-s1*mwgx; cstl[s][1]=c2-s1*mwgy; cstl[s][2]=c3-s1*mbg;
-        cstl[s][3]=s1; cstl[s][4]=c4;
-      }
-    }
-    __syncthreads();
-  }
-  MV5(WQ);
-  for(int s=wid; s<5; s+=4)
-    xg[s][lane]=redp[0][lane][s]+redp[1][lane][s]+redp[2][lane][s]+redp[3][lane][s] + bq2[lane];
   __syncthreads();
-
-  if(!FINAL){
-    const uint4* Ag = (const uint4*)(Aw + ((size_t)b*N_ + chunk*CS_)*64);
-    #pragma unroll
-    for(int jj=0;jj<4;jj++){
-      int f = jj*256 + tid;
-      *(uint4*)(As_ + f*4) = Ag[f];
-    }
-  }
 
   {
     bf16x8 QF0={0,0,0,0,0,0,0,0}, QF1={0,0,0,0,0,0,0,0};
     if(c<5){
-      const float* qpp = &xg[c][0];
+      const float* qpp = qs + (b*K_+c)*64;
       #pragma unroll
       for(int j=0;j<8;j++){
         QF0[j] = (short)f2bf(qpp[q*8+j]);
@@ -564,7 +506,7 @@
         if(lane==0){ rsc[wid][k][0]=scq; rsc[wid][k][1]=As2; rsc[wid][k][2]=Ax2;
                      rsc[wid][k][3]=Ay2; rsc[wid][k][4]=Am2; }
       } else {
-        lgt[(size_t)(bk0+k)*N_ + nrow] = l5[k];
+        lgt[(size_t)(b*K_+k)*N_ + nrow] = l5[k];
         if(lane==0) rsc[wid][k][0]=scq;
       }
     }
@@ -572,7 +514,7 @@
   __syncthreads();
   if(tid<5){
     int k=tid;
-    size_t idx = ((size_t)(bk0+k)*NC_+chunk)*4;
+    size_t idx = ((size_t)(b*K_+k)*NC_+chunk)*4;
     red_out[idx+0]=fmaxf(rm[0][k],rm[1][k]);
     red_out[idx+1]=rsc[0][k][0]+rsc[1][k][0];
     if(FINAL) red_out[idx+2]=fminf(rn[0][k],rn[1][k]);
@@ -617,8 +559,148 @@
       #pragma unroll
       for(int k=0;k<5;k++){
         float s2 = pw[0][k][tid]+pw[1][k][tid]+pw[2][k][tid]+pw[3][k][tid];
-        part_o[((size_t)(bk0+k)*NC_+chunk)*64 + tid] = s2;
-      }
+        part_o[((size_t)(b*K_+k)*NC_+chunk)*64 + tid] = s2;
+      }
+    }
+  }
+
+  if constexpr (GRUTAIL){
+    __shared__ int lastFlag;
+    __syncthreads();
+    if(tid==0){
+      __threadfence();
+      int old = atomicAdd(cnt + b, 1);
+      lastFlag = (old == NC_-1) ? 1 : 0;
+    }
+    __syncthreads();
+    if(lastFlag){
+      __threadfence();
+      __shared__ __align__(16) float sq[5][64];
+      __shared__ float xg[5][64];
+      __shared__ float hg[5][64];
+      __shared__ float redp[4][64][5];
+      __shared__ float lamS[5][NC_];
+      __shared__ float scal4[5][4];
+      int bk0=b*K_;
+      for(int s=wid; s<5; s+=4){
+        size_t base=(size_t)(bk0+s)*NC_;
+        float m_l=(lane<NC_)? red_out[(base+lane)*4]   : -1e30f;
+        float s_l=(lane<NC_)? red_out[(base+lane)*4+1] : 0.f;
+        float M=wmax64(m_l);
+        float eu=(lane<NC_)? __expf(m_l-M) : 0.f;
+        float S=wsum64(s_l*eu);
+        float lam=eu/S;
+        if(lane<NC_) lamS[s][lane]=lam;
+        float p0=(lane<NC_)? pscal_o[(base+lane)*4+0]:0.f;
+        float p1=(lane<NC_)? pscal_o[(base+lane)*4+1]:0.f;
+        float p2=(lane<NC_)? pscal_o[(base+lane)*4+2]:0.f;
+        float p3=(lane<NC_)? pscal_o[(base+lane)*4+3]:0.f;
+        float As=wsum64(lam*p0), Ax=wsum64(lam*p1), Ay=wsum64(lam*p2), Am=wsum64(lam*p3);
+        if(lane==0){ scal4[s][0]=As; scal4[s][1]=Ax; scal4[s][2]=Ay; scal4[s][3]=Am; }
+      }
+      __syncthreads();
+      #pragma unroll
+      for(int s=0;s<5;s++){
+        float p_=0.f;
+        #pragma unroll
+        for(int j=0;j<8;j++){
+          int cc=wid*8+j;
+          p_=fmaf(lamS[s][cc], part_o[((size_t)(bk0+s)*NC_+cc)*64+lane], p_);
+        }
+        redp[wid][lane][s]=p_;
+      }
+      __syncthreads();
+      for(int s=wid; s<5; s+=4)
+        sq[s][lane]=redp[0][lane][s]+redp[1][lane][s]+redp[2][lane][s]+redp[3][lane][s];
+      __syncthreads();
+      MV5(WC);
+      for(int s=wid; s<5; s+=4){
+        float As=scal4[s][0],Ax=scal4[s][1],Ay=scal4[s][2],Am=scal4[s][3];
+        float x_=redp[0][lane][s]+redp[1][lane][s]+redp[2][lane][s]+redp[3][lane][s]
+                + As*uvec[lane] + Ax*uvec[64+lane] + Ay*uvec[128+lane] - Am*uvec[192+lane]
+                + bm2[lane];
+        xg[s][lane]=x_;
+        hg[s][lane]=slot_prev[(bk0+s)*64+lane];
+      }
+      __syncthreads();
+      {
+        float pr[5]={0,0,0,0,0}, pz[5]={0,0,0,0,0}, pi[5]={0,0,0,0,0}, ph[5]={0,0,0,0,0};
+        #pragma unroll
+        for(int dd=0;dd<16;dd++){
+          int d=wid*16+dd;
+          float g0_=gw[d*64+lane],       g1_=gw[4096+d*64+lane],  g2_=gw[8192+d*64+lane];
+          float g3_=gw[12288+d*64+lane], g4_=gw[16384+d*64+lane], g5_=gw[20480+d*64+lane];
+          #pragma unroll
+          for(int s=0;s<5;s++){
+            float xd=xg[s][d], hd=hg[s][d];
+            pr[s]=fmaf(xd,g0_,pr[s]); pr[s]=fmaf(hd,g3_,pr[s]);
+            pz[s]=fmaf(xd,g1_,pz[s]); pz[s]=fmaf(hd,g4_,pz[s]);
+            pi[s]=fmaf(xd,g2_,pi[s]);
+            ph[s]=fmaf(hd,g5_,ph[s]);
+          }
+        }
+        float* redG=(float*)As_;
+        #pragma unroll
+        for(int s=0;s<4;s++){
+          redG[(s*4+0)*256+tid]=pr[s];
+          redG[(s*4+1)*256+tid]=pz[s];
+          redG[(s*4+2)*256+tid]=pi[s];
+          redG[(s*4+3)*256+tid]=ph[s];
+        }
+        redp[wid][lane][0]=pr[4]; redp[wid][lane][1]=pz[4];
+        redp[wid][lane][2]=pi[4]; redp[wid][lane][3]=ph[4];
+      }
+      __syncthreads();
+      for(int s=wid; s<5; s+=4){
+        const float* redG=(const float*)As_;
+        float pr_,pz_,pi_,ph_;
+        if(s<4){
+          int b0=(s*4+0)*256, b1=(s*4+1)*256, b2=(s*4+2)*256, b3=(s*4+3)*256;
+          pr_=redG[b0+lane]+redG[b0+64+lane]+redG[b0+128+lane]+redG[b0+192+lane];
+          pz_=redG[b1+lane]+redG[b1+64+lane]+redG[b1+128+lane]+redG[b1+192+lane];
+          pi_=redG[b2+lane]+redG[b2+64+lane]+redG[b2+128+lane]+redG[b2+192+lane];
+          ph_=redG[b3+lane]+redG[b3+64+lane]+redG[b3+128+lane]+redG[b3+192+lane];
+        } else {
+          pr_=redp[0][lane][0]+redp[1][lane][0]+redp[2][lane][0]+redp[3][lane][0];
+          pz_=redp[0][lane][1]+redp[1][lane][1]+redp[2][lane][1]+redp[3][lane][1];
+          pi_=redp[0][lane][2]+redp[1][lane][2]+redp[2][lane][2]+redp[3][lane][2];
+          ph_=redp[0][lane][3]+redp[1][lane][3]+redp[2][lane][3]+redp[3][lane][3];
+        }
+        float r=1.f/(1.f+__expf(-(pr_+bih[lane]+bhh[lane])));
+        float z=1.f/(1.f+__expf(-(pz_+bih[64+lane]+bhh[64+lane])));
+        float nn=tanhf(pi_+bih[128+lane] + r*(ph_+bhh[128+lane]));
+        float hp=hg[s][lane];
+        float sp=(1.f-z)*nn+z*hp;
+        float m=wsum64(sp)*(1.f/64.f);
+        float df=sp-m;
+        float var=wsum64(df*df)*(1.f/64.f);
+        sq[s][lane]=df*rsqrtf(var+EPS);
+      }
+      __syncthreads();
+      MV5(wrpT);
+      for(int s=wid; s<5; s+=4){
+        float curv=redp[0][lane][s]+redp[1][lane][s]+redp[2][lane][s]+redp[3][lane][s]
+                 + br2[lane] + hg[s][lane];
+        slot_cur[(bk0+s)*64+lane]=curv;
+        float m=wsum64(curv)*(1.f/64.f);
+        float df=curv-m;
+        float var=wsum64(df*df)*(1.f/64.f);
+        float LNc=df*rsqrtf(var+EPS);
+        sq[s][lane]=LNc;
+        float s1=wsum64(LNc*vq[lane])     + csc[0];
+        float c1=wsum64(LNc*vq[64+lane])  + csc[1];
+        float c2=wsum64(LNc*vq[128+lane]) + csc[2];
+        float c3=wsum64(LNc*vq[192+lane]) + csc[3];
+        float c4=wsum64(LNc*vq[256+lane]) + csc[4];
+        if(lane==0){
+          float* cp = cst + (bk0+s)*8;
+          cp[0]=c1-s1*mwgx; cp[1]=c2-s1*mwgy; cp[2]=c3-s1*mbg; cp[3]=s1; cp[4]=c4;
+        }
+      }
+      __syncthreads();
+      MV5(WQ);
+      for(int s=wid; s<5; s+=4)
+        qs[(bk0+s)*64+lane]=redp[0][lane][s]+redp[1][lane][s]+redp[2][lane][s]+redp[3][lane][s] + bq2[lane];
     }
   }
 }
@@ -716,18 +798,17 @@
   float* ws_wgx  = ws_br2 + 64;
   float* ws_wgy  = ws_wgx + 64;
   float* ws_gs   = ws_wgy + 64;
-  float* ws_wqpT = ws_gs + 16;
-  float* ws_wrpT = ws_wqpT + 4096;
-  float* ws_wvT  = ws_wrpT + 4096;
-  float* ws_wmT  = ws_wvT + 4096;
-  float* ws_gw   = ws_wmT + 4096;
+  float* ws_wrpT = ws_gs + 16;
+  float* ws_gw   = ws_wrpT + 4096;
   float* ws_WQ   = ws_gw + 24576;
   float* ws_WC   = ws_WQ + 4096;
   float* ws_bq2  = ws_WC + 4096;
   float* ws_u    = ws_bq2 + 64;
   float* ws_vq   = ws_u + 256;
   float* ws_csc  = ws_vq + 320;
-  float* ws_fc   = ws_csc + 16;
+  float* ws_qs   = ws_csc + 16;
+  float* ws_cst  = ws_qs + B_*K_*D_;
+  float* ws_fc   = ws_cst + 640;
   float* ws_sl0  = ws_fc + (size_t)B_*N_*C_;
   float* ws_sl1  = ws_sl0 + B_*K_*D_;
   float* ws_lgt  = ws_sl1 + B_*K_*D_;
@@ -740,30 +821,31 @@
   float4* ws_kst = (float4*)(ws_psc1 + B_*K_*NC_*4);
   float4* ws_vst = ws_kst + (size_t)B_*N_;
   uint16_t* ws_A = (uint16_t*)(ws_vst + (size_t)B_*N_);
-
-  k_pre<<<189,256,0,stream>>>(mask,noise,mu,lsg, wm,bm,lnkb, wk,wv,lnfb,
+  int* ws_cnt    = (int*)(ws_A + (size_t)B_*N_*64);
+
+  k_pre<<<141,256,0,stream>>>(mask,noise,mu,lsg, wm,bm,lnkb, wk,wv,lnfb,
                               wq,lnqg,lnqb, wres,bres,lnrg,lnrb, wih,whh, wg,bg,
                               lnfg,lnkg,
                               ws_fg,out_fg, ws_bm2,ws_fkb,ws_fvb,ws_qb,ws_br2,
                               ws_wgx,ws_wgy,ws_gs,
-                              ws_wqpT,ws_wrpT,ws_wvT,ws_wmT, ws_gw, ws_sl0, out_slot,
-                              ws_WQ, ws_WC, ws_bq2, ws_u, ws_vq, ws_csc);
+                              ws_wrpT, ws_gw, ws_sl0, out_slot,
+                              ws_WQ, ws_WC, ws_bq2, ws_u, ws_vq, ws_csc, ws_cnt);
   k_featln<<<(B_*N_)/64,256,0,stream>>>(feat,wk,wv,lnfg,ws_fkb,ws_fvb,
                                         ws_wgx,ws_wgy,bg,
                                         featc,lncg,lncb,
                                         ws_A,ws_kst,ws_vst,ws_fc);
 
+  k_slotq0<<<B_*K_,256,0,stream>>>(ws_sl0, ws_WQ,ws_bq2, ws_vq,ws_csc, ws_gs,
+                                   ws_qs, ws_cst);
+
   dim3 agrid(NC_,B_);
-  #define ATT_COMMON ws_A,ws_kst,ws_vst,ws_gs,ws_fg
-  #define ATT_W ws_gw,bih,bhh,ws_wrpT,ws_br2,ws_bm2,ws_WQ,ws_bq2,ws_WC,ws_u,ws_vq,ws_csc
-
-  k_attn<false,false><<<agrid,256,0,stream>>>(ATT_COMMON, ws_sl0, ws_sl1,
-      ws_prt1, ws_psc1, ws_red1, ATT_W, ws_lgt, ws_red0, ws_prt0, ws_psc0);
-  k_attn<true,false><<<agrid,256,0,stream>>>(ATT_COMMON, ws_sl0, ws_sl1,
-      ws_prt0, ws_psc0, ws_red0, ATT_W, ws_lgt, ws_red1, ws_prt1, ws_psc1);
-  k_attn<true,false><<<agrid,256,0,stream>>>(ATT_COMMON, ws_sl1, ws_sl0,
-      ws_prt1, ws_psc1, ws_red1, ATT_W, ws_lgt, ws_red0, ws_prt0, ws_psc0);
-  k_attn<true,true><<<agrid,256,0,stream>>>(ATT_COMMON, ws_sl0, ws_sl1,
-      ws_prt0, ws_psc0, ws_red0, ATT_W, ws_lgt, ws_red1, ws_prt1, ws_psc1);
+  #define AT_ARGS(ROUT,POUT,SCOUT,SPREV,SCUR,CNT) ws_A,ws_kst,ws_vst,ws_qs,ws_cst, \
+      ws_gs,ws_fg, ws_lgt,ROUT,POUT,SCOUT, SPREV,SCUR, \
+      ws_gw,bih,bhh,ws_wrpT,ws_br2,ws_bm2, ws_WQ,ws_bq2, ws_WC,ws_u, ws_vq,ws_csc, CNT
+
+  k_attn<false,true ><<<agrid,256,0,stream>>>(AT_ARGS(ws_red0,ws_prt0,ws_psc0, ws_sl0,ws_sl1, ws_cnt));
+  k_attn<false,true ><<<agrid,256,0,stream>>>(AT_ARGS(ws_red1,ws_prt1,ws_psc1, ws_sl1,ws_sl0, ws_cnt+16));
+  k_attn<false,true ><<<agrid,256,0,stream>>>(AT_ARGS(ws_red0,ws_prt0,ws_psc0, ws_sl0,ws_sl1, ws_cnt+32));
+  k_attn<true ,false><<<agrid,256,0,stream>>>(AT_ARGS(ws_red1,ws_prt1,ws_psc1, ws_sl1,ws_sl1, ws_cnt));
   k_fin<<<dim3(NC_,B_*K_),256,0,stream>>>(ws_lgt,ws_red1,ws_fc,ws_sl1,out_slot,out_attn);
 }
```

Result: slower. 293.2 us (+13.4%).
